# Kernel optimization log

Hardware: AMD Instinct MI355X
Metric: run time of the kernel (lower is better)

## Reference

```python
import jax, jax.numpy as jnp
import numpy as np

K = 4096          # infeatures
N = 4096          # outfeatures (already multiple of 32, padding = 0)
M = 8192
GROUPS = 32       # K / group_size, group_size = 128


def setup_inputs() -> dict:
    key = jax.random.key(0)
    k1, k2, k3, k4, k5, k6 = jax.random.split(key, 6)
    x = jax.random.normal(k1, (M, K), dtype=jnp.float16)
    # packed INT4 weights: 8 nibbles per int32 along the K dimension
    q_weight = jax.random.randint(k2, (K // 8, N), 0, 2**31 - 1, dtype=jnp.int32)
    # packed 4-bit group scales: 8 nibbles per int32 along the N dimension
    q_scale = jax.random.randint(k3, (GROUPS, N // 8), 0, 2**31 - 1, dtype=jnp.int32)
    q_scale_max = (jax.random.uniform(k4, (GROUPS,), dtype=jnp.float32) + 0.5).astype(jnp.float16)
    q_invperm = jax.random.permutation(k5, K).astype(jnp.int32)
    bias = (jax.random.normal(k6, (N,), dtype=jnp.float32) * 0.02).astype(jnp.float16)
    return {"x": x, "q_weight": q_weight, "q_scale": q_scale,
            "q_scale_max": q_scale_max, "q_invperm": q_invperm, "bias": bias}


def _unpack_nibbles(packed, axis):
    # packed int32 -> 8 unsigned 4-bit values expanded along `axis`
    shifts = jnp.arange(8, dtype=jnp.int32) * 4
    shp = [1] * (packed.ndim + 1)
    shp[axis + 1] = 8
    vals = (jnp.expand_dims(packed, axis + 1) >> shifts.reshape(shp)) & 0xF
    out_shape = list(packed.shape)
    out_shape[axis] *= 8
    return vals.reshape(out_shape)


def reference(x, q_weight, q_scale, q_scale_max, q_invperm, bias):
    # --- group-wise INT4 dequantization (EXL2-style scale math) ---
    # per-group/column scale: ((s4 + 1)^2) * (q_scale_max / 256)
    s4 = _unpack_nibbles(q_scale, axis=1).astype(jnp.float16)          # [G, N]
    smax = (q_scale_max.astype(jnp.float32) / 256.0).astype(jnp.float16)
    scale = (s4 + 1.0) * (s4 + 1.0) * smax[:, None]                    # [G, N]
    w4 = _unpack_nibbles(q_weight, axis=0)                              # [K, N], 0..15
    group_size = w4.shape[0] // scale.shape[0]
    scale_rows = jnp.repeat(scale, group_size, axis=0)                  # [K, N]
    W = (w4.astype(jnp.float16) - jnp.float16(8.0)) * scale_rows        # [K, N] fp16
    # --- row permutation fused with GEMM: x is gathered by q_perm ---
    q_perm = jnp.argsort(q_invperm)                                     # [K]
    xp = jnp.take(x.astype(jnp.float16), q_perm, axis=1)                # [M, K]
    out = jnp.matmul(xp, W, preferred_element_type=jnp.float32).astype(jnp.float16)
    out = out + bias
    return out.astype(x.dtype)
```

## Files before the change

### kernel.cpp

```cpp
#include <hip/hip_runtime.h>
#include <stdint.h>

#define K_DIM 4096
#define N_DIM 4096
#define M_DIM 8192

#define BM 256
#define BN 128
#define BK 64
#define NT (K_DIM / BK)

typedef __bf16 bf16x8 __attribute__((ext_vector_type(8)));
typedef float floatx4 __attribute__((ext_vector_type(4)));

__device__ __attribute__((aligned(256))) __bf16 g_Bt[(size_t)N_DIM * K_DIM];
__device__ __attribute__((aligned(256))) __bf16 g_X [(size_t)M_DIM * K_DIM];
__device__ int g_flags[2];

__device__ __forceinline__ void global_to_lds16(const void* g, void* l) {
    __builtin_amdgcn_global_load_lds(
        (const __attribute__((address_space(1))) uint32_t*)g,
        (__attribute__((address_space(3))) uint32_t*)l,
        16, 0, 0);
}

#define LDS_FENCE() asm volatile("" ::: "memory")

__global__ void probe_kernel(const void* xraw, const int* candA, const int* candB) {
    __shared__ int s_insane, s_small, s_badA, s_badB;
    if (threadIdx.x == 0) { s_insane = 0; s_small = 0; s_badA = 0; s_badB = 0; }
    __syncthreads();
    const uint16_t* xw = (const uint16_t*)xraw;
    int insane = 0, small = 0;
    for (int i = threadIdx.x; i < 8192; i += 256) {
        uint16_t a = (uint16_t)(xw[2 * i] & 0x7FFF);
        if (a >= 0x4300) insane++;
        if (a > 0 && a < 0x3000) small++;
    }
    int badA = 0, badB = 0;
    for (int i = threadIdx.x; i < 4096; i += 256) {
        if ((unsigned)candA[i] >= 4096u) badA++;
        if ((unsigned)candB[i] >= 4096u) badB++;
    }
    atomicAdd(&s_insane, insane); atomicAdd(&s_small, small);
    atomicAdd(&s_badA, badA);     atomicAdd(&s_badB, badB);
    __syncthreads();
    if (threadIdx.x == 0) {
        int mode = 0;
        if (s_insane > 32) mode = 1;
        else if (s_small > 100) mode = 2;
        g_flags[0] = mode;
        g_flags[1] = (s_badA > 0 && s_badB == 0) ? 1 : 0;
    }
}

__global__ void __launch_bounds__(256) convert_x_kernel(const void* xraw) {
    const int mode = g_flags[0];
    if (mode == 0) return;
    const size_t nchunk = (size_t)M_DIM * K_DIM / 8;
    for (size_t c = (size_t)blockIdx.x * 256 + threadIdx.x; c < nchunk;
         c += (size_t)gridDim.x * 256) {
        size_t base = c * 8;
        bf16x8 o;
        if (mode == 1) {
            const float* xf = (const float*)xraw;
#pragma unroll
            for (int u = 0; u < 8; ++u) o[u] = (__bf16)xf[base + u];
        } else {
            const _Float16* xh = (const _Float16*)xraw;
#pragma unroll
            for (int u = 0; u < 8; ++u) o[u] = (__bf16)(float)xh[base + u];
        }
        *(bf16x8*)(g_X + base) = o;
    }
}

__global__ void __launch_bounds__(256) dequant_perm_kernel(
    const int* __restrict__ q_weight,
    const int* __restrict__ q_scale,
    const void* __restrict__ qsm_raw,
    const int* __restrict__ candA, const int* __restrict__ candB)
{
    const int mode = g_flags[0];
    const int* q_invperm = g_flags[1] ? candB : candA;

    const int n  = blockIdx.x * 16 + (threadIdx.x & 15);
    const int jp = blockIdx.y * 16 + (threadIdx.x >> 4);
    const int j0 = jp << 3;

    int4 ip0 = *(const int4*)(q_invperm + j0);
    int4 ip1 = *(const int4*)(q_invperm + j0 + 4);
    int ks[8] = {ip0.x, ip0.y, ip0.z, ip0.w, ip1.x, ip1.y, ip1.z, ip1.w};

    const int nshift = (n & 7) << 2;
    const int scol = n >> 3;

    bf16x8 ov;
#pragma unroll
    for (int u = 0; u < 8; ++u) {
        int k = ks[u] & (K_DIM - 1);
        int w4 = (q_weight[(size_t)(k >> 3) * N_DIM + n] >> ((k & 7) << 2)) & 0xF;
        int g = k >> 7;
        int s4 = (q_scale[g * (N_DIM / 8) + scol] >> nshift) & 0xF;
        float smax;
        if (mode == 1)      smax = ((const float*)qsm_raw)[g];
        else if (mode == 2) smax = (float)((const _Float16*)qsm_raw)[g];
        else                smax = (float)((const __bf16*)qsm_raw)[g];
        float sp1 = (float)(s4 + 1);
        float w = (float)(w4 - 8) * (sp1 * sp1 * smax * (1.0f / 256.0f));
        ov[u] = (__bf16)w;
    }
    *(bf16x8*)(g_Bt + (size_t)n * K_DIM + j0) = ov;
}

__global__ void __launch_bounds__(512, 2) gemm_bt_kernel(
    const void* __restrict__ xraw,
    const void* __restrict__ bias_candA, const void* __restrict__ bias_candB,
    void* __restrict__ outraw)
{
    __shared__ __attribute__((aligned(128))) __bf16 sm[3 * BM * BK + 3 * BN * BK];
    const int SB = 3 * BM * BK;

    const int mode = g_flags[0];
    const void* bias_raw = g_flags[1] ? bias_candA : bias_candB;
    const __bf16* __restrict__ Xp = (mode == 0) ? (const __bf16*)xraw : g_X;
    const __bf16* __restrict__ Bt = g_Bt;

    const int tid  = threadIdx.x;
    const int wave = tid >> 6;
    const int lane = tid & 63;

    const int orig = blockIdx.y * 32 + blockIdx.x;
    const int swz  = (orig & 7) * (1024 >> 3) + (orig >> 3);
    const int bn0  = (swz & 31) * BN;
    const int bm0  = (swz >> 5) * BM;

    const int lrow8 = lane >> 3;
    const int ksw   = ((lane & 7) ^ lrow8) << 3;
    const size_t aoff = (size_t)(bm0 + wave * 32 + lrow8) * K_DIM + ksw;
    const size_t boff = (size_t)(bn0 + wave * 16 + lrow8) * K_DIM + ksw;
    const int aldsb = (wave * 4) * 512;
    const int bldsb = (wave * 2) * 512;

    const int wm   = (wave >> 1) << 6;
    const int wn   = (wave & 1) << 6;
    const int frow = lane & 15;
    const int fk   = (lane >> 4) << 3;
    const int ksw8 = (lane & 7) << 3;

    floatx4 acc[4][4] = {};

#pragma unroll
    for (int tt = 0; tt < 2; ++tt) {
#pragma unroll
        for (int c = 0; c < 4; ++c)
            global_to_lds16(Xp + aoff + (size_t)c * (8 * K_DIM) + tt * BK,
                            &sm[tt * (BM * BK) + aldsb + c * 512]);
#pragma unroll
        for (int c = 0; c < 2; ++c)
            global_to_lds16(Bt + boff + (size_t)c * (8 * K_DIM) + tt * BK,
                            &sm[SB + tt * (BN * BK) + bldsb + c * 512]);
    }
    asm volatile("s_waitcnt vmcnt(6)" ::: "memory");
    LDS_FENCE();
    __builtin_amdgcn_s_barrier();
    LDS_FENCE();

    int cur = 0;
#pragma unroll 1
    for (int t = 0; t < NT; ++t) {
        int nb = cur + 2; if (nb >= 3) nb -= 3;
        const int curA = cur * (BM * BK);
        const int curB = SB + cur * (BN * BK);
        const bool stage = (t + 2 < NT);
        const int kt2 = (t + 2) * BK;

#pragma unroll
        for (int ks = 0; ks < 2; ++ks) {
            bf16x8 a[4], b[4];
            const int kb = (ks * 32 + fk) ^ ksw8;
#pragma unroll
            for (int i = 0; i < 4; ++i)
                a[i] = *(const bf16x8*)&sm[curA + (wm + i * 16 + frow) * 64 + kb];
#pragma unroll
            for (int j = 0; j < 4; ++j)
                b[j] = *(const bf16x8*)&sm[curB + (wn + j * 16 + frow) * 64 + kb];

            if (stage) {
                if (ks == 0) {
#pragma unroll
                    for (int c = 0; c < 3; ++c)
                        global_to_lds16(Xp + aoff + (size_t)c * (8 * K_DIM) + kt2,
                                        &sm[nb * (BM * BK) + aldsb + c * 512]);
                } else {
                    global_to_lds16(Xp + aoff + (size_t)3 * (8 * K_DIM) + kt2,
                                    &sm[nb * (BM * BK) + aldsb + 3 * 512]);
#pragma unroll
                    for (int c = 0; c < 2; ++c)
                        global_to_lds16(Bt + boff + (size_t)c * (8 * K_DIM) + kt2,
                                        &sm[SB + nb * (BN * BK) + bldsb + c * 512]);
                }
            }
            if (ks == 1) {
                if (stage) asm volatile("s_waitcnt vmcnt(6)" ::: "memory");
                else       asm volatile("s_waitcnt vmcnt(0)" ::: "memory");
            }
            LDS_FENCE();
            __builtin_amdgcn_s_barrier();
            LDS_FENCE();

            __builtin_amdgcn_s_setprio(1);
#pragma unroll
            for (int i = 0; i < 4; ++i)
#pragma unroll
                for (int j = 0; j < 4; ++j)
                    acc[i][j] = __builtin_amdgcn_mfma_f32_16x16x32_bf16(
                        a[i], b[j], acc[i][j], 0, 0, 0);
            __builtin_amdgcn_s_setprio(0);

            LDS_FENCE();
            __builtin_amdgcn_s_barrier();
            LDS_FENCE();
        }
        cur = cur + 1; if (cur >= 3) cur = 0;
    }

    const int ccol = lane & 15;
    const int crow = (lane >> 4) << 2;
#pragma unroll
    for (int j = 0; j < 4; ++j) {
        const int col = bn0 + wn + j * 16 + ccol;
        float bv;
        if (mode == 1)      bv = ((const float*)bias_raw)[col];
        else if (mode == 2) bv = (float)((const _Float16*)bias_raw)[col];
        else                bv = (float)((const __bf16*)bias_raw)[col];
#pragma unroll
        for (int i = 0; i < 4; ++i) {
            const int row = bm0 + wm + i * 16 + crow;
#pragma unroll
            for (int r = 0; r < 4; ++r) {
                float v = acc[i][j][r] + bv;
                size_t idx = (size_t)(row + r) * N_DIM + col;
                if (mode == 1)      ((float*)outraw)[idx] = v;
                else if (mode == 2) ((_Float16*)outraw)[idx] = (_Float16)v;
                else                ((__bf16*)outraw)[idx] = (__bf16)v;
            }
        }
    }
}

extern "C" void kernel_launch(void* const* d_in, const int* in_sizes, int n_in,
                              void* d_out, int out_size, void* d_ws, size_t ws_size,
                              hipStream_t stream) {
    int idx_x = 0, idx_qw = 1, idx_qs = 2, idx_qsm = 3, idx_a = -1, idx_b = -1;
    for (int i = 0; i < n_in; ++i) {
        switch (in_sizes[i]) {
            case 33554432: idx_x = i; break;
            case 2097152:  idx_qw = i; break;
            case 16384:    idx_qs = i; break;
            case 32:       idx_qsm = i; break;
            case 4096:     (idx_a < 0 ? idx_a : idx_b) = i; break;
            default: break;
        }
    }
    if (idx_a < 0) idx_a = 4;
    if (idx_b < 0) idx_b = 5;

    const void* xraw  = d_in[idx_x];
    const int*  qw    = (const int*)d_in[idx_qw];
    const int*  qs    = (const int*)d_in[idx_qs];
    const void* qsm   = d_in[idx_qsm];
    const int*  candA = (const int*)d_in[idx_a];
    const int*  candB = (const int*)d_in[idx_b];

    probe_kernel<<<1, 256, 0, stream>>>(xraw, candA, candB);
    convert_x_kernel<<<2048, 256, 0, stream>>>(xraw);
    dim3 dqg(N_DIM / 16, (K_DIM / 8) / 16);
    dequant_perm_kernel<<<dqg, 256, 0, stream>>>(qw, qs, qsm, candA, candB);
    dim3 grid(N_DIM / BN, M_DIM / BM);
    gemm_bt_kernel<<<grid, 512, 0, stream>>>(xraw, d_in[idx_a], d_in[idx_b], d_out);
}
```

Before: 546.6 us.

## Use fp16 MFMA directly on fp16 inputs, skip x conversion, coalesce dequant writes

```diff
diff --git a/kernel.cpp b/kernel.cpp
--- a/kernel.cpp
+++ b/kernel.cpp
@@ -11,10 +11,12 @@
 #define NT (K_DIM / BK)
 
 typedef __bf16 bf16x8 __attribute__((ext_vector_type(8)));
+typedef _Float16 f16x8 __attribute__((ext_vector_type(8)));
+typedef unsigned short u16x8 __attribute__((ext_vector_type(8)));
 typedef float floatx4 __attribute__((ext_vector_type(4)));
 
-__device__ __attribute__((aligned(256))) __bf16 g_Bt[(size_t)N_DIM * K_DIM];
-__device__ __attribute__((aligned(256))) __bf16 g_X [(size_t)M_DIM * K_DIM];
+__device__ __attribute__((aligned(256))) unsigned short g_Bt[(size_t)N_DIM * K_DIM];
+__device__ __attribute__((aligned(256))) unsigned short g_X [(size_t)M_DIM * K_DIM];
 __device__ int g_flags[2];
 
 __device__ __forceinline__ void global_to_lds16(const void* g, void* l) {
@@ -55,23 +57,25 @@
 }
 
 __global__ void __launch_bounds__(256) convert_x_kernel(const void* xraw) {
-    const int mode = g_flags[0];
-    if (mode == 0) return;
+    if (g_flags[0] != 1) return;
     const size_t nchunk = (size_t)M_DIM * K_DIM / 8;
+    const float* xf = (const float*)xraw;
     for (size_t c = (size_t)blockIdx.x * 256 + threadIdx.x; c < nchunk;
          c += (size_t)gridDim.x * 256) {
         size_t base = c * 8;
-        bf16x8 o;
-        if (mode == 1) {
-            const float* xf = (const float*)xraw;
-#pragma unroll
-            for (int u = 0; u < 8; ++u) o[u] = (__bf16)xf[base + u];
-        } else {
-            const _Float16* xh = (const _Float16*)xraw;
-#pragma unroll
-            for (int u = 0; u < 8; ++u) o[u] = (__bf16)(float)xh[base + u];
-        }
-        *(bf16x8*)(g_X + base) = o;
+        float4 v0 = *(const float4*)(xf + base);
+        float4 v1 = *(const float4*)(xf + base + 4);
+        u16x8 o;
+        _Float16 h;
+        h = (_Float16)v0.x; o[0] = __builtin_bit_cast(unsigned short, h);
+        h = (_Float16)v0.y; o[1] = __builtin_bit_cast(unsigned short, h);
+        h = (_Float16)v0.z; o[2] = __builtin_bit_cast(unsigned short, h);
+        h = (_Float16)v0.w; o[3] = __builtin_bit_cast(unsigned short, h);
+        h = (_Float16)v1.x; o[4] = __builtin_bit_cast(unsigned short, h);
+        h = (_Float16)v1.y; o[5] = __builtin_bit_cast(unsigned short, h);
+        h = (_Float16)v1.z; o[6] = __builtin_bit_cast(unsigned short, h);
+        h = (_Float16)v1.w; o[7] = __builtin_bit_cast(unsigned short, h);
+        *(u16x8*)(g_X + base) = o;
     }
 }
 
@@ -81,12 +85,15 @@
     const void* __restrict__ qsm_raw,
     const int* __restrict__ candA, const int* __restrict__ candB)
 {
+    __shared__ __attribute__((aligned(16))) unsigned short lds[16 * 136];
+
     const int mode = g_flags[0];
     const int* q_invperm = g_flags[1] ? candB : candA;
 
-    const int n  = blockIdx.x * 16 + (threadIdx.x & 15);
-    const int jp = blockIdx.y * 16 + (threadIdx.x >> 4);
-    const int j0 = jp << 3;
+    const int n_l  = threadIdx.x & 15;
+    const int jp_l = threadIdx.x >> 4;
+    const int n  = blockIdx.x * 16 + n_l;
+    const int j0 = (blockIdx.y * 16 + jp_l) << 3;
 
     int4 ip0 = *(const int4*)(q_invperm + j0);
     int4 ip1 = *(const int4*)(q_invperm + j0 + 4);
@@ -95,7 +102,7 @@
     const int nshift = (n & 7) << 2;
     const int scol = n >> 3;
 
-    bf16x8 ov;
+    u16x8 ov;
 #pragma unroll
     for (int u = 0; u < 8; ++u) {
         int k = ks[u] & (K_DIM - 1);
@@ -108,23 +115,35 @@
         else                smax = (float)((const __bf16*)qsm_raw)[g];
         float sp1 = (float)(s4 + 1);
         float w = (float)(w4 - 8) * (sp1 * sp1 * smax * (1.0f / 256.0f));
-        ov[u] = (__bf16)w;
-    }
-    *(bf16x8*)(g_Bt + (size_t)n * K_DIM + j0) = ov;
-}
-
+        if (mode != 0) { _Float16 h = (_Float16)w; ov[u] = __builtin_bit_cast(unsigned short, h); }
+        else           { __bf16   b = (__bf16)w;   ov[u] = __builtin_bit_cast(unsigned short, b); }
+    }
+    *(u16x8*)&lds[n_l * 136 + jp_l * 8] = ov;
+    __syncthreads();
+
+    const int row = threadIdx.x >> 4;
+    const int c16 = threadIdx.x & 15;
+    u16x8 t = *(const u16x8*)&lds[row * 136 + c16 * 8];
+    *(u16x8*)(g_Bt + (size_t)(blockIdx.x * 16 + row) * K_DIM
+              + (size_t)blockIdx.y * 128 + c16 * 8) = t;
+}
+
+template <bool F16>
 __global__ void __launch_bounds__(512, 2) gemm_bt_kernel(
     const void* __restrict__ xraw,
     const void* __restrict__ bias_candA, const void* __restrict__ bias_candB,
     void* __restrict__ outraw)
 {
-    __shared__ __attribute__((aligned(128))) __bf16 sm[3 * BM * BK + 3 * BN * BK];
+    const int mode = g_flags[0];
+    if (F16 != (mode != 0)) return;
+
+    __shared__ __attribute__((aligned(128))) unsigned short sm[3 * BM * BK + 3 * BN * BK];
     const int SB = 3 * BM * BK;
 
-    const int mode = g_flags[0];
     const void* bias_raw = g_flags[1] ? bias_candA : bias_candB;
-    const __bf16* __restrict__ Xp = (mode == 0) ? (const __bf16*)xraw : g_X;
-    const __bf16* __restrict__ Bt = g_Bt;
+    const unsigned short* __restrict__ Xp =
+        (mode == 1) ? g_X : (const unsigned short*)xraw;
+    const unsigned short* __restrict__ Bt = g_Bt;
 
     const int tid  = threadIdx.x;
     const int wave = tid >> 6;
@@ -177,14 +196,14 @@
 
 #pragma unroll
         for (int ks = 0; ks < 2; ++ks) {
-            bf16x8 a[4], b[4];
+            u16x8 a[4], b[4];
             const int kb = (ks * 32 + fk) ^ ksw8;
 #pragma unroll
             for (int i = 0; i < 4; ++i)
-                a[i] = *(const bf16x8*)&sm[curA + (wm + i * 16 + frow) * 64 + kb];
+                a[i] = *(const u16x8*)&sm[curA + (wm + i * 16 + frow) * 64 + kb];
 #pragma unroll
             for (int j = 0; j < 4; ++j)
-                b[j] = *(const bf16x8*)&sm[curB + (wn + j * 16 + frow) * 64 + kb];
+                b[j] = *(const u16x8*)&sm[curB + (wn + j * 16 + frow) * 64 + kb];
 
             if (stage) {
                 if (ks == 0) {
@@ -213,9 +232,16 @@
 #pragma unroll
             for (int i = 0; i < 4; ++i)
 #pragma unroll
-                for (int j = 0; j < 4; ++j)
-                    acc[i][j] = __builtin_amdgcn_mfma_f32_16x16x32_bf16(
-                        a[i], b[j], acc[i][j], 0, 0, 0);
+                for (int j = 0; j < 4; ++j) {
+                    if constexpr (F16)
+                        acc[i][j] = __builtin_amdgcn_mfma_f32_16x16x32_f16(
+                            __builtin_bit_cast(f16x8, a[i]),
+                            __builtin_bit_cast(f16x8, b[j]), acc[i][j], 0, 0, 0);
+                    else
+                        acc[i][j] = __builtin_amdgcn_mfma_f32_16x16x32_bf16(
+                            __builtin_bit_cast(bf16x8, a[i]),
+                            __builtin_bit_cast(bf16x8, b[j]), acc[i][j], 0, 0, 0);
+                }
             __builtin_amdgcn_s_setprio(0);
 
             LDS_FENCE();
@@ -278,5 +304,6 @@
     dim3 dqg(N_DIM / 16, (K_DIM / 8) / 16);
     dequant_perm_kernel<<<dqg, 256, 0, stream>>>(qw, qs, qsm, candA, candB);
     dim3 grid(N_DIM / BN, M_DIM / BM);
-    gemm_bt_kernel<<<grid, 512, 0, stream>>>(xraw, d_in[idx_a], d_in[idx_b], d_out);
-}
+    gemm_bt_kernel<true ><<<grid, 512, 0, stream>>>(xraw, d_in[idx_a], d_in[idx_b], d_out);
+    gemm_bt_kernel<false><<<grid, 512, 0, stream>>>(xraw, d_in[idx_a], d_in[idx_b], d_out);
+}
```

After: 547.7 us. About the same (+0.2%).
